# Performance work log

Measured on AMD Instinct MI355X. Metric: run time of the kernel, lower is better.

## Reference

```python
import jax, jax.numpy as jnp
import numpy as np

N = 100000      # nodes
E = 1600000     # edges
IN, H, OUT = 128, 128, 64
FUSION_W = 0.5


def setup_inputs() -> dict:
    key = jax.random.key(0)
    ks = jax.random.split(key, 10)
    x = jax.random.normal(ks[0], (N, IN), dtype=jnp.float32)
    edge_index = jax.random.randint(ks[1], (2, E), 0, N, dtype=jnp.int32)

    def lin(k, fi, fo):
        return jax.random.normal(k, (fi, fo), dtype=jnp.float32) / np.float32(np.sqrt(fi))

    return {
        "x": x,
        "edge_index": edge_index,
        "gnn_W1": lin(ks[2], IN, H),  "gnn_b1": jnp.zeros((H,), jnp.float32),
        "gnn_W2": lin(ks[3], H, OUT), "gnn_b2": jnp.zeros((OUT,), jnp.float32),
        "mlp_W1": lin(ks[4], IN, H),  "mlp_b1": jnp.zeros((H,), jnp.float32),
        "mlp_W2": lin(ks[5], H, OUT), "mlp_b2": jnp.zeros((OUT,), jnp.float32),
    }


def _gcn_conv(x, W, b, src, dst, deg_inv_sqrt, deg_inv):
    # GCNConv: x' = D^{-1/2} (A + I) D^{-1/2} (x W) + b, deg counts self-loops
    h = x @ W                                     # [N, F_out]
    norm = deg_inv_sqrt[src] * deg_inv_sqrt[dst]  # [E]
    agg = jax.ops.segment_sum(h[src] * norm[:, None], dst, num_segments=N)
    # self-loop contribution has norm 1/deg
    return agg + h * deg_inv[:, None] + b


def reference(x, edge_index, gnn_W1, gnn_b1, gnn_W2, gnn_b2,
              mlp_W1, mlp_b1, mlp_W2, mlp_b2):
    src, dst = edge_index[0], edge_index[1]
    # in-degree including self-loops (PyG GCNConv default add_self_loops=True)
    deg = 1.0 + jax.ops.segment_sum(jnp.ones((E,), jnp.float32), dst, num_segments=N)
    deg_inv_sqrt = jax.lax.rsqrt(deg)
    deg_inv = 1.0 / deg

    # GNN branch (dropout is identity in eval mode)
    h = jax.nn.relu(_gcn_conv(x, gnn_W1, gnn_b1, src, dst, deg_inv_sqrt, deg_inv))
    z_gnn = _gcn_conv(h, gnn_W2, gnn_b2, src, dst, deg_inv_sqrt, deg_inv)

    # MLP branch
    z_mlp = jax.nn.relu(x @ mlp_W1 + mlp_b1) @ mlp_W2 + mlp_b2

    return FUSION_W * z_gnn + (1.0 - FUSION_W) * z_mlp
```

## Files before the change

### kernel.cpp

```cpp
#include <hip/hip_runtime.h>
#include <hip/hip_fp16.h>

static constexpr int IN_F = 128;
static constexpr int FCAP = 6144;

typedef _Float16 half8 __attribute__((ext_vector_type(8)));
typedef _Float16 half4 __attribute__((ext_vector_type(4)));
typedef float f32x4 __attribute__((ext_vector_type(4)));
typedef float f32x2 __attribute__((ext_vector_type(2)));

__device__ inline void acc_fp8x8(uint2 u, f32x2* a) {
    a[0] += __builtin_amdgcn_cvt_pk_f32_fp8(u.x, false);
    a[1] += __builtin_amdgcn_cvt_pk_f32_fp8(u.x, true);
    a[2] += __builtin_amdgcn_cvt_pk_f32_fp8(u.y, false);
    a[3] += __builtin_amdgcn_cvt_pk_f32_fp8(u.y, true);
}
__device__ inline void acc_fp8x4(unsigned u, f32x2* a) {
    a[0] += __builtin_amdgcn_cvt_pk_f32_fp8(u, false);
    a[1] += __builtin_amdgcn_cvt_pk_f32_fp8(u, true);
}
__device__ inline void fp8x8_to_f32(uint2 u, float* f) {
    f32x2 a0 = __builtin_amdgcn_cvt_pk_f32_fp8(u.x, false);
    f32x2 a1 = __builtin_amdgcn_cvt_pk_f32_fp8(u.x, true);
    f32x2 a2 = __builtin_amdgcn_cvt_pk_f32_fp8(u.y, false);
    f32x2 a3 = __builtin_amdgcn_cvt_pk_f32_fp8(u.y, true);
    f[0] = a0[0]; f[1] = a0[1]; f[2] = a1[0]; f[3] = a1[1];
    f[4] = a2[0]; f[5] = a2[1]; f[6] = a3[0]; f[7] = a3[1];
}
__device__ inline void fp8x4_to_f32(unsigned u, float* f) {
    f32x2 a0 = __builtin_amdgcn_cvt_pk_f32_fp8(u, false);
    f32x2 a1 = __builtin_amdgcn_cvt_pk_f32_fp8(u, true);
    f[0] = a0[0]; f[1] = a0[1]; f[2] = a1[0]; f[3] = a1[1];
}
__device__ inline unsigned char f32_to_fp8(float v) {
    return (unsigned char)__builtin_amdgcn_cvt_pk_fp8_f32(v, v, 0, false);
}


__global__ __launch_bounds__(1024) void kb_count(const int* __restrict__ dst,
                                                 int* __restrict__ bcount, int E) {
    __shared__ int cnt[16][512];
    const int tid = threadIdx.x;
    const int wv  = tid >> 6;
    for (int i = tid; i < 16 * 512; i += 1024) (&cnt[0][0])[i] = 0;
    __syncthreads();
#pragma unroll
    for (int q = 0; q < 8; ++q) {
        int i = blockIdx.x * 8192 + q * 1024 + tid;
        if (i < E) atomicAdd(&cnt[wv][dst[i] >> 8], 1);
    }
    __syncthreads();
    if (tid < 512) {
        int run = 0;
#pragma unroll
        for (int w = 0; w < 16; ++w) run += cnt[w][tid];
        if (run > 0) atomicAdd(&bcount[tid], run);
    }
}

__global__ __launch_bounds__(512) void k_scanb(const int* __restrict__ bcount,
                                               int* __restrict__ bbase,
                                               int* __restrict__ bcursor, int NB) {
    __shared__ int s[512];
    const int tid = threadIdx.x;
    int v = (tid < NB) ? bcount[tid] : 0;
    s[tid] = v;
    __syncthreads();
    int inc = v;
#pragma unroll
    for (int off = 1; off < 512; off <<= 1) {
        int add = (tid >= off) ? s[tid - off] : 0;
        __syncthreads();
        s[tid] = inc = inc + add;
        __syncthreads();
    }
    if (tid < NB) { bbase[tid] = inc - v; bcursor[tid] = inc - v; }
    if (tid == NB - 1) bbase[NB] = inc;
}

__global__ __launch_bounds__(1024) void kb_move(const int* __restrict__ src,
                                                const int* __restrict__ dst,
                                                int* __restrict__ bcursor,
                                                unsigned* __restrict__ recs, int E) {
    __shared__ int cnt[16][512];
    __shared__ int gbase[512];
    const int tid = threadIdx.x;
    const int wv  = tid >> 6;
    for (int i = tid; i < 16 * 512; i += 1024) (&cnt[0][0])[i] = 0;
    __syncthreads();

    int bq[8];
    unsigned rq[8];
#pragma unroll
    for (int q = 0; q < 8; ++q) {
        int i = blockIdx.x * 8192 + q * 1024 + tid;
        if (i < E) {
            int d = dst[i];
            int s = src[i];
            bq[q] = d >> 8;
            rq[q] = (unsigned)(((d & 255) << 17) | s);
            atomicAdd(&cnt[wv][bq[q]], 1);
        } else {
            bq[q] = -1;
            rq[q] = 0u;
        }
    }
    __syncthreads();
    if (tid < 512) {
        int run = 0;
#pragma unroll
        for (int w = 0; w < 16; ++w) {
            int t = cnt[w][tid];
            cnt[w][tid] = run;
            run += t;
        }
        gbase[tid] = (run > 0) ? atomicAdd(&bcursor[tid], run) : 0;
    }
    __syncthreads();
#pragma unroll
    for (int q = 0; q < 8; ++q) {
        if (bq[q] >= 0) {
            int p = gbase[bq[q]] + atomicAdd(&cnt[wv][bq[q]], 1);
            recs[p] = rq[q];
        }
    }
}

__global__ __launch_bounds__(512) void kb_fill_lds(const unsigned* __restrict__ recs,
                                                   const int* __restrict__ bbase,
                                                   int* __restrict__ row_ptr,
                                                   float* __restrict__ dis,
                                                   int* __restrict__ csr, int n, int E) {
    __shared__ int hist[2048];
    __shared__ int wsum[512];
    __shared__ int base[2048];
    __shared__ int cur[2048];
    __shared__ int stage[FCAP];
    const int tid   = threadIdx.x;
    const int b     = blockIdx.x;
    const int s     = bbase[b], e = bbase[b + 1];
    const int nbase = b << 8;

    for (int i = tid; i < 2048; i += 512) hist[i] = 0;
    __syncthreads();
    for (int i = s + tid; i < e; i += 512) {
        unsigned r = recs[i];
        int dl = (int)(r >> 17);
        int sr = (int)(r & 0x1FFFFu);
        atomicAdd(&hist[(dl << 3) | (sr >> 14)], 1);
    }
    __syncthreads();

    const int l0 = hist[tid * 4 + 0];
    const int l1 = hist[tid * 4 + 1];
    const int l2 = hist[tid * 4 + 2];
    const int l3 = hist[tid * 4 + 3];
    const int tot = l0 + l1 + l2 + l3;
    wsum[tid] = tot;
    __syncthreads();
    int inc = tot;
#pragma unroll
    for (int off = 1; off < 512; off <<= 1) {
        int add = (tid >= off) ? wsum[tid - off] : 0;
        __syncthreads();
        wsum[tid] = inc = inc + add;
        __syncthreads();
    }
    int run = inc - tot;
    base[tid * 4 + 0] = run; cur[tid * 4 + 0] = 0; run += l0;
    base[tid * 4 + 1] = run; cur[tid * 4 + 1] = 0; run += l1;
    base[tid * 4 + 2] = run; cur[tid * 4 + 2] = 0; run += l2;
    base[tid * 4 + 3] = run; cur[tid * 4 + 3] = 0; run += l3;
    __syncthreads();

    if (tid < 256) {
        int cnt = 0;
#pragma unroll
        for (int q = 0; q < 8; ++q) cnt += hist[tid * 8 + q];
        const int idx = nbase + tid;
        if (idx < n) {
            row_ptr[idx] = s + base[tid * 8];
            dis[idx] = rsqrtf(1.0f + (float)cnt);
        }
        if (idx == n) row_ptr[n] = s + base[tid * 8];
        if (tid == 255 && nbase + 256 == n) row_ptr[n] = e;
    }
    __syncthreads();

    for (int i = s + tid; i < e; i += 512) {
        unsigned r = recs[i];
        int dl = (int)(r >> 17);
        int sr = (int)(r & 0x1FFFFu);
        int k  = (dl << 3) | (sr >> 14);
        int slot = base[k] + atomicAdd(&cur[k], 1);
        if (slot < FCAP) stage[slot] = sr;
        else csr[s + slot] = sr;
    }
    __syncthreads();

    const int total = e - s;
    const int lim = total < FCAP ? total : FCAP;
    for (int i = tid; i < lim; i += 512)
        csr[s + i] = stage[i];
}

__global__ __launch_bounds__(256) void k_prep_w(const float* __restrict__ gW1,
                                                const float* __restrict__ mW1,
                                                const float* __restrict__ mW2,
                                                const float* __restrict__ gW2,
                                                _Float16* __restrict__ tg1,
                                                _Float16* __restrict__ tm1,
                                                _Float16* __restrict__ tm2,
                                                _Float16* __restrict__ tg2) {
    int i = blockIdx.x * 256 + threadIdx.x;
    if (i < 16384)      { int j = i;         int f = j >> 7, k = j & 127; tg1[j] = (_Float16)gW1[k * 128 + f]; }
    else if (i < 32768) { int j = i - 16384; int f = j >> 7, k = j & 127; tm1[j] = (_Float16)mW1[k * 128 + f]; }
    else if (i < 40960) { int j = i - 32768; int f = j >> 7, k = j & 127; tm2[j] = (_Float16)mW2[k * 64 + f]; }
    else if (i < 49152) { int j = i - 40960; int f = j >> 7, k = j & 127; tg2[j] = (_Float16)gW2[k * 64 + f]; }
}

__global__ __launch_bounds__(256) void k_dual_mfma(const float* __restrict__ x,
                                                   const _Float16* __restrict__ tg1,
                                                   const _Float16* __restrict__ tm1,
                                                   const _Float16* __restrict__ tm2,
                                                   const float* __restrict__ b1,
                                                   const float* __restrict__ b2,
                                                   const float* __restrict__ dis,
                                                   unsigned char* __restrict__ h1,
                                                   _Float16* __restrict__ z, int nrows) {
    __shared__ _Float16 As[64 * 128];
    __shared__ _Float16 Ws[64 * 128];
    _Float16* Ms = As;
    const int tid  = threadIdx.x;
    const int row0 = blockIdx.x * 64;

#pragma unroll
    for (int p = 0; p < 4; ++p) {
        int sid = p * 256 + tid;
        int r = sid >> 4, s = sid & 15;
        int gr = row0 + r;
        uint4 v = make_uint4(0, 0, 0, 0);
        if (gr < nrows) {
            const float4 f0 = *reinterpret_cast<const float4*>(x + (size_t)gr * 128 + s * 8);
            const float4 f1 = *reinterpret_cast<const float4*>(x + (size_t)gr * 128 + s * 8 + 4);
            _Float16 t[8] = {(_Float16)f0.x, (_Float16)f0.y, (_Float16)f0.z, (_Float16)f0.w,
                             (_Float16)f1.x, (_Float16)f1.y, (_Float16)f1.z, (_Float16)f1.w};
            v = *reinterpret_cast<uint4*>(t);
        }
        *reinterpret_cast<uint4*>(&As[r * 128 + ((s ^ (r & 7)) * 8)]) = v;
    }

    const int lane = tid & 63;
    const int wv   = tid >> 6;
    const int mrow = wv * 16 + (lane & 15);
    const int kg   = lane >> 4;
    const int grow = row0 + wv * 16 + kg * 4;

    auto stageW = [&](const _Float16* Wt, int wbase) {
#pragma unroll
        for (int p = 0; p < 4; ++p) {
            int sid = p * 256 + tid;
            int r = sid >> 4, s = sid & 15;
            uint4 v = *reinterpret_cast<const uint4*>(Wt + (size_t)(wbase + r) * 128 + s * 8);
            *reinterpret_cast<uint4*>(&Ws[r * 128 + ((s ^ (r & 7)) * 8)]) = v;
        }
    };

    stageW(tg1, 0);
    __syncthreads();

    half8 a[4];
#pragma unroll
    for (int kk = 0; kk < 4; ++kk)
        a[kk] = *reinterpret_cast<const half8*>(&As[mrow * 128 + (((kk * 4 + kg) ^ (mrow & 7)) * 8)]);

    float dvals[4];
#pragma unroll
    for (int j = 0; j < 4; ++j)
        dvals[j] = (grow + j < nrows) ? dis[grow + j] : 0.f;

#pragma unroll
    for (int half = 0; half < 2; ++half) {
        if (half == 1) {
            __syncthreads();
            stageW(tg1, 64);
            __syncthreads();
        }
#pragma unroll
        for (int ct = 0; ct < 4; ++ct) {
            const int ncol = half * 64 + ct * 16 + (lane & 15);
            const int wrow = ncol & 63;
            f32x4 acc = {0.f, 0.f, 0.f, 0.f};
#pragma unroll
            for (int kk = 0; kk < 4; ++kk) {
                half8 b = *reinterpret_cast<const half8*>(&Ws[wrow * 128 + (((kk * 4 + kg) ^ (wrow & 7)) * 8)]);
                acc = __builtin_amdgcn_mfma_f32_16x16x32_f16(a[kk], b, acc, 0, 0, 0);
            }
#pragma unroll
            for (int j = 0; j < 4; ++j)
                if (grow + j < nrows)
                    h1[(size_t)(grow + j) * 128 + ncol] = f32_to_fp8(acc[j] * dvals[j]);
        }
    }
    __syncthreads();

#pragma unroll
    for (int half = 0; half < 2; ++half) {
        stageW(tm1, half * 64);
        __syncthreads();
#pragma unroll
        for (int ct = 0; ct < 4; ++ct) {
            const int ncol = half * 64 + ct * 16 + (lane & 15);
            const int wrow = ncol & 63;
            f32x4 acc = {0.f, 0.f, 0.f, 0.f};
#pragma unroll
            for (int kk = 0; kk < 4; ++kk) {
                half8 b = *reinterpret_cast<const half8*>(&Ws[wrow * 128 + (((kk * 4 + kg) ^ (wrow & 7)) * 8)]);
                acc = __builtin_amdgcn_mfma_f32_16x16x32_f16(a[kk], b, acc, 0, 0, 0);
            }
            const float bias = b1[ncol];
#pragma unroll
            for (int j = 0; j < 4; ++j) {
                int r = wv * 16 + kg * 4 + j;
                float v = fmaxf((float)acc[j] + bias, 0.f);
                Ms[r * 128 + (((ncol >> 3) ^ (r & 7)) * 8) + (ncol & 7)] = (_Float16)v;
            }
        }
        __syncthreads();
    }

    stageW(tm2, 0);
    __syncthreads();

    half8 am[4];
#pragma unroll
    for (int kk = 0; kk < 4; ++kk)
        am[kk] = *reinterpret_cast<const half8*>(&Ms[mrow * 128 + (((kk * 4 + kg) ^ (mrow & 7)) * 8)]);

#pragma unroll
    for (int ct = 0; ct < 4; ++ct) {
        const int ncol = ct * 16 + (lane & 15);
        f32x4 acc = {0.f, 0.f, 0.f, 0.f};
#pragma unroll
        for (int kk = 0; kk < 4; ++kk) {
            half8 b = *reinterpret_cast<const half8*>(&Ws[ncol * 128 + (((kk * 4 + kg) ^ (ncol & 7)) * 8)]);
            acc = __builtin_amdgcn_mfma_f32_16x16x32_f16(am[kk], b, acc, 0, 0, 0);
        }
        const float bias = b2[ncol];
#pragma unroll
        for (int j = 0; j < 4; ++j)
            if (grow + j < nrows)
                z[(size_t)(grow + j) * 64 + ncol] = (_Float16)((float)acc[j] + bias);
    }
}

__global__ __launch_bounds__(256) void k_mm64(const _Float16* __restrict__ A,
                                              const _Float16* __restrict__ Wt,
                                              const float* __restrict__ dis,
                                              unsigned char* __restrict__ C, int nrows) {
    __shared__ _Float16 As[64 * 128];
    __shared__ _Float16 Ws[64 * 128];
    const int tid  = threadIdx.x;
    const int row0 = blockIdx.x * 64;

#pragma unroll
    for (int p = 0; p < 4; ++p) {
        int sid = p * 256 + tid;
        int r = sid >> 4, s = sid & 15;
        int gr = row0 + r;
        uint4 v = make_uint4(0, 0, 0, 0);
        if (gr < nrows) v = *reinterpret_cast<const uint4*>(A + (size_t)gr * 128 + s * 8);
        *reinterpret_cast<uint4*>(&As[r * 128 + ((s ^ (r & 7)) * 8)]) = v;
    }
#pragma unroll
    for (int p = 0; p < 4; ++p) {
        int sid = p * 256 + tid;
        int r = sid >> 4, s = sid & 15;
        uint4 v = *reinterpret_cast<const uint4*>(Wt + (size_t)r * 128 + s * 8);
        *reinterpret_cast<uint4*>(&Ws[r * 128 + ((s ^ (r & 7)) * 8)]) = v;
    }
    __syncthreads();

    const int lane = tid & 63;
    const int wv   = tid >> 6;
    const int mrow = wv * 16 + (lane & 15);
    const int kg   = lane >> 4;
    const int grow = row0 + wv * 16 + kg * 4;

    half8 a[4];
#pragma unroll
    for (int kk = 0; kk < 4; ++kk)
        a[kk] = *reinterpret_cast<const half8*>(&As[mrow * 128 + (((kk * 4 + kg) ^ (mrow & 7)) * 8)]);

    float dvals[4];
#pragma unroll
    for (int j = 0; j < 4; ++j)
        dvals[j] = (grow + j < nrows) ? dis[grow + j] : 0.f;

#pragma unroll
    for (int ct = 0; ct < 4; ++ct) {
        const int ncol = ct * 16 + (lane & 15);
        f32x4 acc = {0.f, 0.f, 0.f, 0.f};
#pragma unroll
        for (int kk = 0; kk < 4; ++kk) {
            half8 b = *reinterpret_cast<const half8*>(&Ws[ncol * 128 + (((kk * 4 + kg) ^ (ncol & 7)) * 8)]);
            acc = __builtin_amdgcn_mfma_f32_16x16x32_f16(a[kk], b, acc, 0, 0, 0);
        }
#pragma unroll
        for (int j = 0; j < 4; ++j)
            if (grow + j < nrows)
                C[(size_t)(grow + j) * 64 + ncol] = f32_to_fp8(acc[j] * dvals[j]);
    }
}

__global__ __launch_bounds__(256) void k_agg1(const int* __restrict__ rp,
                                              const int* __restrict__ csr,
                                              const float* __restrict__ dis,
                                              const unsigned char* __restrict__ h1,
                                              const float* __restrict__ b,
                                              _Float16* __restrict__ out, int n) {
    const int tid  = threadIdx.x;
    const int node = blockIdx.x * 16 + (tid >> 4);
    if (node >= n) return;
    const int c0 = (tid & 15) * 8;
    const int start = rp[node], end = rp[node + 1];

    f32x2 acc[4] = {{0.f, 0.f}, {0.f, 0.f}, {0.f, 0.f}, {0.f, 0.f}};

    int j = start;
    for (; j + 1 < end; j += 2) {
        int s0 = csr[j];
        int s1 = csr[j + 1];
        uint2 u0 = *reinterpret_cast<const uint2*>(h1 + (size_t)s0 * 128 + c0);
        uint2 u1 = *reinterpret_cast<const uint2*>(h1 + (size_t)s1 * 128 + c0);
        acc_fp8x8(u0, acc);
        acc_fp8x8(u1, acc);
    }
    if (j < end) {
        int s0 = csr[j];
        uint2 u0 = *reinterpret_cast<const uint2*>(h1 + (size_t)s0 * 128 + c0);
        acc_fp8x8(u0, acc);
    }

    const float dd = dis[node];
    uint2 un = *reinterpret_cast<const uint2*>(h1 + (size_t)node * 128 + c0);
    float fn[8];
    fp8x8_to_f32(un, fn);
    const float av[8] = {acc[0][0], acc[0][1], acc[1][0], acc[1][1],
                         acc[2][0], acc[2][1], acc[3][0], acc[3][1]};
    const float4 bv0 = *reinterpret_cast<const float4*>(b + c0);
    const float4 bv1 = *reinterpret_cast<const float4*>(b + c0 + 4);
    const float bb[8] = {bv0.x, bv0.y, bv0.z, bv0.w, bv1.x, bv1.y, bv1.z, bv1.w};
    half8 o;
#pragma unroll
    for (int k = 0; k < 8; ++k)
        o[k] = (_Float16)fmaxf(dd * (av[k] + fn[k]) + bb[k], 0.f);
    *reinterpret_cast<half8*>(out + (size_t)node * 128 + c0) = o;
}

__global__ __launch_bounds__(256) void k_agg2(const int* __restrict__ rp,
                                              const int* __restrict__ csr,
                                              const float* __restrict__ dis,
                                              const unsigned char* __restrict__ h2,
                                              const float* __restrict__ b,
                                              const _Float16* __restrict__ zmlp,
                                              float* __restrict__ out, int n) {
    const int tid  = threadIdx.x;
    const int node = blockIdx.x * 16 + (tid >> 4);
    if (node >= n) return;
    const int c0 = (tid & 15) * 4;
    const int start = rp[node], end = rp[node + 1];

    f32x2 acc[2] = {{0.f, 0.f}, {0.f, 0.f}};

    int j = start;
    for (; j + 1 < end; j += 2) {
        int s0 = csr[j];
        int s1 = csr[j + 1];
        unsigned u0 = *reinterpret_cast<const unsigned*>(h2 + (size_t)s0 * 64 + c0);
        unsigned u1 = *reinterpret_cast<const unsigned*>(h2 + (size_t)s1 * 64 + c0);
        acc_fp8x4(u0, acc);
        acc_fp8x4(u1, acc);
    }
    if (j < end) {
        int s0 = csr[j];
        unsigned u0 = *reinterpret_cast<const unsigned*>(h2 + (size_t)s0 * 64 + c0);
        acc_fp8x4(u0, acc);
    }

    const float dd = dis[node];
    unsigned un = *reinterpret_cast<const unsigned*>(h2 + (size_t)node * 64 + c0);
    float fn[4];
    fp8x4_to_f32(un, fn);
    const float av[4] = {acc[0][0], acc[0][1], acc[1][0], acc[1][1]};
    half4 zm = *reinterpret_cast<const half4*>(zmlp + (size_t)node * 64 + c0);
    const float4 bv = *reinterpret_cast<const float4*>(b + c0);
    const float bb[4] = {bv.x, bv.y, bv.z, bv.w};
    float4 o;
    float* op = &o.x;
#pragma unroll
    for (int k = 0; k < 4; ++k)
        op[k] = 0.5f * ((dd * (av[k] + fn[k]) + bb[k]) + (float)zm[k]);
    *reinterpret_cast<float4*>(out + (size_t)node * 64 + c0) = o;
}

extern "C" void kernel_launch(void* const* d_in, const int* in_sizes, int n_in,
                              void* d_out, int out_size, void* d_ws, size_t ws_size,
                              hipStream_t stream) {
    const float* x      = (const float*)d_in[0];
    const int* edge_idx = (const int*)d_in[1];
    const float* gnn_W1 = (const float*)d_in[2];
    const float* gnn_b1 = (const float*)d_in[3];
    const float* gnn_W2 = (const float*)d_in[4];
    const float* gnn_b2 = (const float*)d_in[5];
    const float* mlp_W1 = (const float*)d_in[6];
    const float* mlp_b1 = (const float*)d_in[7];
    const float* mlp_W2 = (const float*)d_in[8];
    const float* mlp_b2 = (const float*)d_in[9];
    float* out = (float*)d_out;

    const int N = in_sizes[0] / IN_F;
    const int E = in_sizes[1] / 2;
    const int* src = edge_idx;
    const int* dst = edge_idx + E;

    const int NB = (N + 255) >> 8;

    char* wp = (char*)d_ws;
    int* row_ptr   = (int*)wp;            wp += ((size_t)N + 4) * sizeof(int);
    int* bbase     = (int*)wp;            wp += 516 * sizeof(int);
    int* bcursor   = (int*)wp;            wp += 512 * sizeof(int);
    int* bcount    = (int*)wp;            wp += 512 * sizeof(int);
    int* csr       = (int*)wp;            wp += (size_t)E * sizeof(int);
    unsigned* recs = (unsigned*)wp;       wp += (size_t)E * sizeof(unsigned);
    float* dis     = (float*)wp;          wp += (size_t)N * sizeof(float);
    _Float16* tg1  = (_Float16*)wp;       wp += 16384 * sizeof(_Float16);
    _Float16* tm1  = (_Float16*)wp;       wp += 16384 * sizeof(_Float16);
    _Float16* tm2  = (_Float16*)wp;       wp += 8192 * sizeof(_Float16);
    _Float16* tg2  = (_Float16*)wp;       wp += 8192 * sizeof(_Float16);
    unsigned char* h1 = (unsigned char*)wp;  wp += (size_t)N * 128;
    _Float16* hmid = (_Float16*)wp;       wp += (size_t)N * 128 * sizeof(_Float16);
    unsigned char* h2 = (unsigned char*)wp;  wp += (size_t)N * 64;
    wp = (char*)(((uintptr_t)wp + 15) & ~(uintptr_t)15);
    _Float16* zmlp = (_Float16*)wp;       wp += (size_t)N * 64 * sizeof(_Float16);

    k_prep_w<<<192, 256, 0, stream>>>(gnn_W1, mlp_W1, mlp_W2, gnn_W2, tg1, tm1, tm2, tg2);

    hipMemsetAsync(bcount, 0, 512 * sizeof(int), stream);
    const int mvblocks = (E + 8191) / 8192;
    kb_count<<<mvblocks, 1024, 0, stream>>>(dst, bcount, E);
    k_scanb<<<1, 512, 0, stream>>>(bcount, bbase, bcursor, NB);
    kb_move<<<mvblocks, 1024, 0, stream>>>(src, dst, bcursor, recs, E);
    kb_fill_lds<<<NB, 512, 0, stream>>>(recs, bbase, row_ptr, dis, csr, N, E);

    const int gblocks = (N + 63) / 64;
    const int ablocks = (N + 15) / 16;

    k_dual_mfma<<<gblocks, 256, 0, stream>>>(x, tg1, tm1, tm2, mlp_b1, mlp_b2, dis, h1, zmlp, N);

    k_agg1<<<ablocks, 256, 0, stream>>>(row_ptr, csr, dis, h1, gnn_b1, hmid, N);

    k_mm64<<<gblocks, 256, 0, stream>>>(hmid, tg2, dis, h2, N);

    k_agg2<<<ablocks, 256, 0, stream>>>(row_ptr, csr, dis, h2, gnn_b2, zmlp, out, N);
}
```

Baseline: 182.7 us.

## Split each node's edge list across four lane groups in aggregation kernels

Both aggregation kernels now give each node a full 64-lane wavefront instead of 16 lanes. Four 16-lane groups each walk an interleaved quarter of the neighbor list, unrolled by four, and the partial sums are combined with cross-lane shuffles before group 0 writes the result. This shortens each node's serial gather chain and raises memory-level parallelism for the random feature loads, which suits an average degree of about 16. In exchange it launches four times as many blocks, adds shuffle reductions, and leaves lanes idle for low-degree nodes.

Measured after the change: 197.8 us. 8.3% more time.

```diff
diff --git a/kernel.cpp b/kernel.cpp
--- a/kernel.cpp
+++ b/kernel.cpp
@@ -420,42 +420,58 @@
                                               const float* __restrict__ b,
                                               _Float16* __restrict__ out, int n) {
     const int tid  = threadIdx.x;
-    const int node = blockIdx.x * 16 + (tid >> 4);
+    const int node = blockIdx.x * 4 + (tid >> 6);
     if (node >= n) return;
-    const int c0 = (tid & 15) * 8;
+    const int lane = tid & 63;
+    const int g    = lane >> 4;
+    const int c0   = (lane & 15) * 8;
     const int start = rp[node], end = rp[node + 1];
 
     f32x2 acc[4] = {{0.f, 0.f}, {0.f, 0.f}, {0.f, 0.f}, {0.f, 0.f}};
 
-    int j = start;
-    for (; j + 1 < end; j += 2) {
+    int j = start + g;
+    for (; j + 12 < end; j += 16) {
         int s0 = csr[j];
-        int s1 = csr[j + 1];
+        int s1 = csr[j + 4];
+        int s2 = csr[j + 8];
+        int s3 = csr[j + 12];
         uint2 u0 = *reinterpret_cast<const uint2*>(h1 + (size_t)s0 * 128 + c0);
         uint2 u1 = *reinterpret_cast<const uint2*>(h1 + (size_t)s1 * 128 + c0);
+        uint2 u2 = *reinterpret_cast<const uint2*>(h1 + (size_t)s2 * 128 + c0);
+        uint2 u3 = *reinterpret_cast<const uint2*>(h1 + (size_t)s3 * 128 + c0);
         acc_fp8x8(u0, acc);
         acc_fp8x8(u1, acc);
-    }
-    if (j < end) {
+        acc_fp8x8(u2, acc);
+        acc_fp8x8(u3, acc);
+    }
+    for (; j < end; j += 4) {
         int s0 = csr[j];
         uint2 u0 = *reinterpret_cast<const uint2*>(h1 + (size_t)s0 * 128 + c0);
         acc_fp8x8(u0, acc);
     }
 
-    const float dd = dis[node];
-    uint2 un = *reinterpret_cast<const uint2*>(h1 + (size_t)node * 128 + c0);
-    float fn[8];
-    fp8x8_to_f32(un, fn);
-    const float av[8] = {acc[0][0], acc[0][1], acc[1][0], acc[1][1],
-                         acc[2][0], acc[2][1], acc[3][0], acc[3][1]};
-    const float4 bv0 = *reinterpret_cast<const float4*>(b + c0);
-    const float4 bv1 = *reinterpret_cast<const float4*>(b + c0 + 4);
-    const float bb[8] = {bv0.x, bv0.y, bv0.z, bv0.w, bv1.x, bv1.y, bv1.z, bv1.w};
-    half8 o;
-#pragma unroll
-    for (int k = 0; k < 8; ++k)
-        o[k] = (_Float16)fmaxf(dd * (av[k] + fn[k]) + bb[k], 0.f);
-    *reinterpret_cast<half8*>(out + (size_t)node * 128 + c0) = o;
+    float av[8] = {acc[0][0], acc[0][1], acc[1][0], acc[1][1],
+                   acc[2][0], acc[2][1], acc[3][0], acc[3][1]};
+#pragma unroll
+    for (int k = 0; k < 8; ++k) {
+        av[k] += __shfl_xor(av[k], 16);
+        av[k] += __shfl_xor(av[k], 32);
+    }
+
+    if (g == 0) {
+        const float dd = dis[node];
+        uint2 un = *reinterpret_cast<const uint2*>(h1 + (size_t)node * 128 + c0);
+        float fn[8];
+        fp8x8_to_f32(un, fn);
+        const float4 bv0 = *reinterpret_cast<const float4*>(b + c0);
+        const float4 bv1 = *reinterpret_cast<const float4*>(b + c0 + 4);
+        const float bb[8] = {bv0.x, bv0.y, bv0.z, bv0.w, bv1.x, bv1.y, bv1.z, bv1.w};
+        half8 o;
+#pragma unroll
+        for (int k = 0; k < 8; ++k)
+            o[k] = (_Float16)fmaxf(dd * (av[k] + fn[k]) + bb[k], 0.f);
+        *reinterpret_cast<half8*>(out + (size_t)node * 128 + c0) = o;
+    }
 }
 
 __global__ __launch_bounds__(256) void k_agg2(const int* __restrict__ rp,
@@ -466,42 +482,58 @@
                                               const _Float16* __restrict__ zmlp,
                                               float* __restrict__ out, int n) {
     const int tid  = threadIdx.x;
-    const int node = blockIdx.x * 16 + (tid >> 4);
+    const int node = blockIdx.x * 4 + (tid >> 6);
     if (node >= n) return;
-    const int c0 = (tid & 15) * 4;
+    const int lane = tid & 63;
+    const int g    = lane >> 4;
+    const int c0   = (lane & 15) * 4;
     const int start = rp[node], end = rp[node + 1];
 
     f32x2 acc[2] = {{0.f, 0.f}, {0.f, 0.f}};
 
-    int j = start;
-    for (; j + 1 < end; j += 2) {
+    int j = start + g;
+    for (; j + 12 < end; j += 16) {
         int s0 = csr[j];
-        int s1 = csr[j + 1];
+        int s1 = csr[j + 4];
+        int s2 = csr[j + 8];
+        int s3 = csr[j + 12];
         unsigned u0 = *reinterpret_cast<const unsigned*>(h2 + (size_t)s0 * 64 + c0);
         unsigned u1 = *reinterpret_cast<const unsigned*>(h2 + (size_t)s1 * 64 + c0);
+        unsigned u2 = *reinterpret_cast<const unsigned*>(h2 + (size_t)s2 * 64 + c0);
+        unsigned u3 = *reinterpret_cast<const unsigned*>(h2 + (size_t)s3 * 64 + c0);
         acc_fp8x4(u0, acc);
         acc_fp8x4(u1, acc);
-    }
-    if (j < end) {
+        acc_fp8x4(u2, acc);
+        acc_fp8x4(u3, acc);
+    }
+    for (; j < end; j += 4) {
         int s0 = csr[j];
         unsigned u0 = *reinterpret_cast<const unsigned*>(h2 + (size_t)s0 * 64 + c0);
         acc_fp8x4(u0, acc);
     }
 
-    const float dd = dis[node];
-    unsigned un = *reinterpret_cast<const unsigned*>(h2 + (size_t)node * 64 + c0);
-    float fn[4];
-    fp8x4_to_f32(un, fn);
-    const float av[4] = {acc[0][0], acc[0][1], acc[1][0], acc[1][1]};
-    half4 zm = *reinterpret_cast<const half4*>(zmlp + (size_t)node * 64 + c0);
-    const float4 bv = *reinterpret_cast<const float4*>(b + c0);
-    const float bb[4] = {bv.x, bv.y, bv.z, bv.w};
-    float4 o;
-    float* op = &o.x;
-#pragma unroll
-    for (int k = 0; k < 4; ++k)
-        op[k] = 0.5f * ((dd * (av[k] + fn[k]) + bb[k]) + (float)zm[k]);
-    *reinterpret_cast<float4*>(out + (size_t)node * 64 + c0) = o;
+    float av[4] = {acc[0][0], acc[0][1], acc[1][0], acc[1][1]};
+#pragma unroll
+    for (int k = 0; k < 4; ++k) {
+        av[k] += __shfl_xor(av[k], 16);
+        av[k] += __shfl_xor(av[k], 32);
+    }
+
+    if (g == 0) {
+        const float dd = dis[node];
+        unsigned un = *reinterpret_cast<const unsigned*>(h2 + (size_t)node * 64 + c0);
+        float fn[4];
+        fp8x4_to_f32(un, fn);
+        half4 zm = *reinterpret_cast<const half4*>(zmlp + (size_t)node * 64 + c0);
+        const float4 bv = *reinterpret_cast<const float4*>(b + c0);
+        const float bb[4] = {bv.x, bv.y, bv.z, bv.w};
+        float4 o;
+        float* op = &o.x;
+#pragma unroll
+        for (int k = 0; k < 4; ++k)
+            op[k] = 0.5f * ((dd * (av[k] + fn[k]) + bb[k]) + (float)zm[k]);
+        *reinterpret_cast<float4*>(out + (size_t)node * 64 + c0) = o;
+    }
 }
 
 extern "C" void kernel_launch(void* const* d_in, const int* in_sizes, int n_in,
@@ -554,7 +586,7 @@
     kb_fill_lds<<<NB, 512, 0, stream>>>(recs, bbase, row_ptr, dis, csr, N, E);
 
     const int gblocks = (N + 63) / 64;
-    const int ablocks = (N + 15) / 16;
+    const int ablocks = (N + 3) / 4;
 
     k_dual_mfma<<<gblocks, 256, 0, stream>>>(x, tg1, tm1, tm2, mlp_b1, mlp_b2, dis, h1, zmlp, N);
 
```
